# Optimization experiments

Hardware: AMD Instinct MI355X
Metric: run time of the kernel (lower is better)

## Reference

```python
import jax, jax.numpy as jnp
import numpy as np

DIM = 1024
HEADS = 16
DIM_HEAD = 64
INNER = HEADS * DIM_HEAD
B, N = 2, 2048


def rope_encoding(seq_len, dim_head):
    inv_freq = 1.0 / (10000.0 ** (jnp.arange(0, dim_head, 2, dtype=jnp.float32) / dim_head))
    pos = jnp.arange(seq_len, dtype=jnp.float32)
    sinusoid = pos[:, None] * inv_freq[None, :]          # [n, d/2]
    return jnp.concatenate([jnp.sin(sinusoid), jnp.cos(sinusoid)], axis=-1)  # [n, d]


def setup_inputs() -> dict:
    key = jax.random.key(0)
    k1, k2, k3, k4 = jax.random.split(key, 4)
    feats = jax.random.normal(k1, (B, N, DIM), dtype=jnp.float32)
    mask = jnp.ones((B, N), dtype=bool)
    # params (torch Linear: y = x @ W.T + b; store as [in, out] for x @ W)
    W_qkv = jax.random.normal(k2, (DIM, 3 * INNER), dtype=jnp.float32) / np.sqrt(DIM)
    W_out = jax.random.normal(k3, (INNER, DIM), dtype=jnp.float32) / np.sqrt(INNER)
    b_out = jax.random.normal(k4, (DIM,), dtype=jnp.float32) * 0.01
    return {"feats": feats, "W_qkv": W_qkv, "W_out": W_out, "b_out": b_out, "mask": mask}


def reference(feats, W_qkv, W_out, b_out, mask):
    b, n, _ = feats.shape
    h, d = HEADS, DIM_HEAD
    scale = d ** -0.5

    qkv = feats @ W_qkv                                   # [b, n, 3*inner]
    q, k, v = jnp.split(qkv, 3, axis=-1)
    to_bhnd = lambda t: t.reshape(b, n, h, d).transpose(0, 2, 1, 3)
    q, k, v = to_bhnd(q), to_bhnd(k), to_bhnd(v)          # [b, h, n, d]

    rope = rope_encoding(n, d)                            # [n, d]
    q = q + rope
    k = k + rope

    m = mask[:, None, :, None]                            # [b, 1, n, 1]
    neg_max = -jnp.finfo(k.dtype).max
    k = jnp.where(m, k, neg_max)

    q = jax.nn.softmax(q, axis=-1)                        # over feature dim
    k = jax.nn.softmax(k, axis=-2)                        # over sequence dim
    q = q * scale
    v = jnp.where(m, v, 0.0)

    context = jnp.einsum('bhnd,bhne->bhde', k, v)         # [b, h, d, d]
    out = jnp.einsum('bhde,bhnd->bhne', context, q)       # [b, h, n, d]
    out = out.transpose(0, 2, 1, 3).reshape(b, n, h * d)  # [b, n, inner]
    out = out @ W_out + b_out                             # [b, n, dim]

    attn = jnp.einsum('bhnd,bhmd->bhnm', q, k) * scale    # [b, h, n, n]
    return out, attn
```

## Files before the change

### kernel.cpp

```cpp
#include <hip/hip_runtime.h>
#include <cstddef>


#define BB     2
#define SEQ    2048
#define DIMM   1024
#define NHEADS 16
#define DH     64
#define TRIPLE 3072
#define ROWS   (BB*SEQ)
#define SCALE  0.125f

typedef unsigned short u16;
typedef unsigned int   u32;
typedef short s16x8 __attribute__((ext_vector_type(8)));
typedef float f32x4 __attribute__((ext_vector_type(4)));
typedef float vf4   __attribute__((ext_vector_type(4)));

static constexpr size_t WS_QB    = 0;
static constexpr size_t WS_KB    = 8388608;
static constexpr size_t WS_DEN   = 16777216;
static constexpr size_t WS_CTX   = 16785408;
static constexpr size_t WS_ROPET = 17309696;
static constexpr size_t WS_OPPK  = 17833984;
static constexpr size_t WS_WOPK  = 34611200;

static constexpr size_t SC_QKV  = 0;
static constexpr size_t SC_APK  = 50331648;
static constexpr size_t SC_WQPK = 67108864;

__device__ __forceinline__ u16 f2bf(float x) {
    u32 u = __float_as_uint(x);
    return (u16)((u + 0x7fffu + ((u >> 16) & 1u)) >> 16);
}
__device__ __forceinline__ float bf2f(u16 h) {
    return __uint_as_float(((u32)h) << 16);
}
__device__ __forceinline__ void glds16(const char* g, char* l) {
    __builtin_amdgcn_global_load_lds(
        (const __attribute__((address_space(1))) void*)g,
        (__attribute__((address_space(3))) void*)l, 16, 0, 0);
}

__device__ __forceinline__ void conv_pack_item(const float* __restrict__ src,
                                               u16* __restrict__ dst, int t)
{
    int g  = t & 3;
    int kb = (t >> 2) & 31;
    int row = t >> 7;
    const float* s = src + (size_t)row * 1024 + kb * 32 + 4 * g;
    float4 xa = *(const float4*)s;
    float4 xb = *(const float4*)(s + 16);
    float xs[8] = {xa.x, xa.y, xa.z, xa.w, xb.x, xb.y, xb.z, xb.w};
    s16x8 hv, lv;
    #pragma unroll
    for (int e = 0; e < 8; ++e) {
        u16 h = f2bf(xs[e]);
        hv[e] = (short)h;
        lv[e] = (short)f2bf(xs[e] - bf2f(h));
    }
    size_t rowc = (size_t)row * 256 + kb * 8;
    int sw = row & 7;
    *(s16x8*)(dst + (rowc + (size_t)(g ^ sw)) * 8)       = hv;
    *(s16x8*)(dst + (rowc + (size_t)((4 | g) ^ sw)) * 8) = lv;
}

__device__ __forceinline__ void conv_packT_tile(const float* __restrict__ W,
                                                u16* __restrict__ dst, int N,
                                                int n0, int kb, int t,
                                                float (*fb)[128])
{
    int k0 = kb * 32;
    #pragma unroll
    for (int q = 0; q < 4; ++q) {
        int cc = q * 256 + t;
        int kr = cc >> 5, nc = (cc & 31) * 4;
        *(float4*)&fb[kr][nc] = *(const float4*)&W[(size_t)(k0 + kr) * N + n0 + nc];
    }
    __syncthreads();
    #pragma unroll
    for (int it = 0; it < 2; ++it) {
        int item = it * 256 + t;
        int g = (item >> 7) & 3, n = item & 127;
        s16x8 hv, lv;
        #pragma unroll
        for (int e = 0; e < 4; ++e) {
            float x0 = fb[4 * g + e][n];
            float x1 = fb[16 + 4 * g + e][n];
            u16 h0 = f2bf(x0), h1 = f2bf(x1);
            hv[e]     = (short)h0;
            hv[e + 4] = (short)h1;
            lv[e]     = (short)f2bf(x0 - bf2f(h0));
            lv[e + 4] = (short)f2bf(x1 - bf2f(h1));
        }
        int row = n0 + n;
        size_t rowc = (size_t)row * 256 + kb * 8;
        int sw = row & 7;
        *(s16x8*)(dst + (rowc + (size_t)(g ^ sw)) * 8)       = hv;
        *(s16x8*)(dst + (rowc + (size_t)((4 | g) ^ sw)) * 8) = lv;
    }
}

__global__ __launch_bounds__(256)
void prologue(float4* __restrict__ denctx, float4* __restrict__ ropeT,
              const float* __restrict__ feats, u16* __restrict__ A_pk,
              const float* __restrict__ Wqkv, u16* __restrict__ Wq_pk,
              const float* __restrict__ Wout, u16* __restrict__ Wo_pk)
{
    __shared__ float fb[32][128];
    const int bid = blockIdx.x, tid = threadIdx.x;
    if (bid < 130) {
        denctx[bid * 256 + tid] = float4{0.f, 0.f, 0.f, 0.f};
        return;
    }
    if (bid < 258) {
        int t = (bid - 130) * 256 + tid;
        int pos = t >> 4, r16 = t & 15;
        double a0 = (double)pos * pow(10000.0, -(double)r16 / 32.0);
        double a1 = (double)pos * pow(10000.0, -(double)(r16 + 16) / 32.0);
        float4 v;
        v.x = (float)sin(a0); v.y = (float)sin(a1);
        v.z = (float)cos(a0); v.w = (float)cos(a1);
        ropeT[t] = v;
        return;
    }
    if (bid < 2306) {
        conv_pack_item(feats, A_pk, (bid - 258) * 256 + tid);
        return;
    }
    if (bid < 3074) {
        int cb = bid - 2306;
        conv_packT_tile(Wqkv, Wq_pk, TRIPLE, (cb % 24) * 128, cb / 24, tid, fb);
        return;
    }
    {
        int cb = bid - 3074;
        conv_packT_tile(Wout, Wo_pk, DIMM, (cb & 7) * 128, cb >> 3, tid, fb);
    }
}

__global__ __launch_bounds__(256, 3)
void gemm_qkv(const u16* __restrict__ Ap, const u16* __restrict__ Bp,
              float* __restrict__ C, const float* __restrict__ ropeT,
              float* __restrict__ den)
{
    __shared__ __align__(16) char smem[32768];
    const int tid = threadIdx.x;
    const int lane = tid & 63, wid = tid >> 6;
    const int wi = wid >> 1, wj = wid & 1;
    const int r16 = lane & 15, g = lane >> 4;

    const int bid = blockIdx.x;
    const int swz = (bid & 7) * 96 + (bid >> 3);
    const int bx = swz % 24, by = swz / 24;
    const int brow = by * 128, bcol = bx * 128;

    const int srow = wid * 32 + (lane >> 3);
    const int sch  = lane & 7;
    const char* gA = (const char*)Ap + ((size_t)(brow + srow) * 256 + sch) * 16;
    const char* gB = (const char*)Bp + ((size_t)(bcol + srow) * 256 + sch) * 16;
    char* la = smem + wid * 4096;
    char* lb = smem + 16384 + wid * 4096;

    f32x4 acc[4][4] = {};
    size_t koff = 0;
    for (int kb = 0; kb < 32; ++kb, koff += 128) {
        #pragma unroll
        for (int q = 0; q < 4; ++q) {
            glds16(gA + (size_t)q * (8 * 4096) + koff, la + q * 1024);
            glds16(gB + (size_t)q * (8 * 4096) + koff, lb + q * 1024);
        }
        __syncthreads();
        s16x8 ah[4], al[4], bh[4], bl[4];
        #pragma unroll
        for (int i = 0; i < 4; ++i) {
            int ra = wi * 64 + i * 16 + r16;
            const s16x8* Ar = (const s16x8*)(smem + (size_t)ra * 128);
            ah[i] = Ar[g ^ (ra & 7)];
            al[i] = Ar[(4 | g) ^ (ra & 7)];
            int rb = wj * 64 + i * 16 + r16;
            const s16x8* Br = (const s16x8*)(smem + 16384 + (size_t)rb * 128);
            bh[i] = Br[g ^ (rb & 7)];
            bl[i] = Br[(4 | g) ^ (rb & 7)];
        }
        #pragma unroll
        for (int i = 0; i < 4; ++i)
            #pragma unroll
            for (int j = 0; j < 4; ++j) {
                acc[i][j] = __builtin_amdgcn_mfma_f32_16x16x32_bf16(ah[i], bh[j], acc[i][j], 0, 0, 0);
                acc[i][j] = __builtin_amdgcn_mfma_f32_16x16x32_bf16(ah[i], bl[j], acc[i][j], 0, 0, 0);
                acc[i][j] = __builtin_amdgcn_mfma_f32_16x16x32_bf16(al[i], bh[j], acc[i][j], 0, 0, 0);
            }
        __syncthreads();
    }

    const int pos0 = brow & (SEQ - 1);
    const vf4* rT = (const vf4*)ropeT;
    if (bx < 8) {
        #pragma unroll
        for (int i = 0; i < 4; ++i)
            #pragma unroll
            for (int r = 0; r < 4; ++r) {
                int rloc = wi * 64 + i * 16 + g * 4 + r;
                vf4 rv = rT[(size_t)(pos0 + rloc) * 16 + r16];
                float v[4];
                #pragma unroll
                for (int j = 0; j < 4; ++j) v[j] = acc[i][j][r] + rv[j];
                float m = fmaxf(fmaxf(v[0], v[1]), fmaxf(v[2], v[3]));
                #pragma unroll
                for (int o = 1; o <= 8; o <<= 1) m = fmaxf(m, __shfl_xor(m, o));
                float e[4];
                float s = 0.f;
                #pragma unroll
                for (int j = 0; j < 4; ++j) { e[j] = expf(v[j] - m); s += e[j]; }
                #pragma unroll
                for (int o = 1; o <= 8; o <<= 1) s += __shfl_xor(s, o);
                float inv = SCALE / s;
                size_t rb = (size_t)(brow + rloc) * TRIPLE + bcol + wj * 64;
                #pragma unroll
                for (int j = 0; j < 4; ++j)
                    C[rb + j * 16 + r16] = e[j] * inv;
            }
    } else if (bx < 16) {
        float dsum[4] = {0.f, 0.f, 0.f, 0.f};
        #pragma unroll
        for (int i = 0; i < 4; ++i)
            #pragma unroll
            for (int r = 0; r < 4; ++r) {
                int rloc = wi * 64 + i * 16 + g * 4 + r;
                vf4 rv = rT[(size_t)(pos0 + rloc) * 16 + r16];
                size_t rb = (size_t)(brow + rloc) * TRIPLE + bcol + wj * 64;
                #pragma unroll
                for (int j = 0; j < 4; ++j) {
                    float e = expf(acc[i][j][r] + rv[j]);
                    C[rb + j * 16 + r16] = e;
                    dsum[j] += e;
                }
            }
        const int bD = (brow >> 11) * DIMM;
        #pragma unroll
        for (int j = 0; j < 4; ++j) {
            float s = dsum[j];
            s += __shfl_xor(s, 16);
            s += __shfl_xor(s, 32);
            if (g == 0)
                atomicAdd(&den[bD + (bcol - DIMM) + wj * 64 + j * 16 + r16], s);
        }
    } else {
        #pragma unroll
        for (int i = 0; i < 4; ++i) {
            int row = brow + wi * 64 + i * 16 + g * 4;
            #pragma unroll
            for (int j = 0; j < 4; ++j) {
                int col = bcol + wj * 64 + j * 16 + r16;
                #pragma unroll
                for (int r = 0; r < 4; ++r)
                    C[(size_t)(row + r) * TRIPLE + col] = acc[i][j][r];
            }
        }
    }
}

__global__ __launch_bounds__(256)
void packctx(const float* __restrict__ qkv, const float* __restrict__ den,
             u16* __restrict__ qb, u16* __restrict__ kb, float* __restrict__ ctx)
{
    __shared__ float kt[32][64];
    __shared__ float vt[32][64];
    if (blockIdx.x < 2048) {
        int t = blockIdx.x * 256 + threadIdx.x;
        int g  = t & 3;
        int db = (t >> 2) & 1;
        int h  = (t >> 3) & 15;
        int row = t >> 7;
        int b = row >> 11, n = row & (SEQ - 1);
        size_t dst = ((size_t)(b * NHEADS + h) * SEQ + n) * 64 + db * 32 + g * 8;
        const float* sq = qkv + (size_t)row * TRIPLE + h * DH + db * 32 + 4 * g;
        {
            float4 xa = *(const float4*)sq;
            float4 xb = *(const float4*)(sq + 16);
            float xs[8] = {xa.x, xa.y, xa.z, xa.w, xb.x, xb.y, xb.z, xb.w};
            s16x8 hv;
            #pragma unroll
            for (int e = 0; e < 8; ++e) hv[e] = (short)f2bf(xs[e]);
            *(s16x8*)(qb + dst) = hv;
        }
        {
            const float* sk = sq + DIMM;
            const float* dn = den + (size_t)b * DIMM + h * DH + db * 32 + 4 * g;
            float4 xa = *(const float4*)sk;
            float4 xb = *(const float4*)(sk + 16);
            float4 da = *(const float4*)dn;
            float4 dc = *(const float4*)(dn + 16);
            float xs[8] = {xa.x / da.x, xa.y / da.y, xa.z / da.z, xa.w / da.w,
                           xb.x / dc.x, xb.y / dc.y, xb.z / dc.z, xb.w / dc.w};
            s16x8 hv;
            #pragma unroll
            for (int e = 0; e < 8; ++e) hv[e] = (short)f2bf(xs[e]);
            *(s16x8*)(kb + dst) = hv;
        }
        return;
    }
    int cb = blockIdx.x - 2048;
    int chunk = cb & 7, h = (cb >> 3) & 15, b = cb >> 7;
    int row0 = b * SEQ + chunk * 256;
    int d  = threadIdx.x & 63;
    int eg = threadIdx.x >> 6;
    float acc[16] = {};
    for (int t = 0; t < 8; ++t) {
        #pragma unroll
        for (int q = 0; q < 2; ++q) {
            int lf = threadIdx.x * 2 + q;
            int nn = lf >> 4;
            int c4 = (lf & 15) * 4;
            size_t base = (size_t)(row0 + t * 32 + nn) * TRIPLE + DIMM + h * DH + c4;
            *(float4*)&kt[nn][c4] = *(const float4*)&qkv[base];
            *(float4*)&vt[nn][c4] = *(const float4*)&qkv[base + DIMM];
        }
        __syncthreads();
        #pragma unroll 8
        for (int nn = 0; nn < 32; ++nn) {
            float kv = kt[nn][d];
            #pragma unroll
            for (int j = 0; j < 16; ++j)
                acc[j] = fmaf(kv, vt[nn][eg * 16 + j], acc[j]);
        }
        __syncthreads();
    }
    float rden = 1.f / den[(size_t)b * DIMM + h * DH + d];
    size_t cbase = ((size_t)(b * NHEADS + h)) * (DH * DH) + d * DH + eg * 16;
    #pragma unroll
    for (int j = 0; j < 16; ++j) atomicAdd(&ctx[cbase + j], acc[j] * rden);
}

__global__ __launch_bounds__(256)
void outpre(const float* __restrict__ qkv, const float* __restrict__ ctx,
            u16* __restrict__ op_pk)
{
    int h = blockIdx.y, b = blockIdx.z;
    int row0 = b * SEQ + blockIdx.x * 64;
    __shared__ float cl[64][64];
    __shared__ float ql[4][64];
    const float* C = ctx + ((size_t)(b * NHEADS + h)) * (DH * DH);
    for (int i = threadIdx.x; i < DH * DH; i += 256) cl[i >> 6][i & 63] = C[i];
    __syncthreads();
    int w = threadIdx.x >> 6, lane = threadIdx.x & 63;
    const int m    = lane & 31;
    const int kbI  = h * 2 + (lane >> 5);
    const int g2   = (m & 15) >> 2;
    const int elem = (m & 3) | ((m >> 4) << 2);
    for (int it = 0; it < 16; ++it) {
        int row = row0 + w * 16 + it;
        float qv = qkv[(size_t)row * TRIPLE + h * DH + lane];
        ql[w][lane] = qv;
        float acc = 0.f;
        #pragma unroll
        for (int d = 0; d < 64; ++d) acc = fmaf(cl[d][lane], ql[w][d], acc);
        u16 hi = f2bf(acc);
        u16 lo = f2bf(acc - bf2f(hi));
        int sw = row & 7;
        size_t base = (size_t)row * 2048 + (size_t)kbI * 64;
        op_pk[base + ((g2 ^ sw) * 8 + elem)]       = hi;
        op_pk[base + (((4 | g2) ^ sw) * 8 + elem)] = lo;
    }
}

__global__ __launch_bounds__(256, 2)
void epilogue2(const u16* __restrict__ Op_pk, const u16* __restrict__ Wo_pk,
               float* __restrict__ outp, const float* __restrict__ bias,
               const u16* __restrict__ qb, const u16* __restrict__ kb,
               float* __restrict__ attn)
{
    __shared__ __align__(16) char smem[65536];
    const int tid = threadIdx.x;
    const int lane = tid & 63, wid = tid >> 6;
    const int r16 = lane & 15, g = lane >> 4;
    const int bid = blockIdx.x;

    if (bid % 17 == 0) {
        const int gb = bid / 17;
        const int wi = wid >> 1, wj = wid & 1;
        const int swz = (gb & 7) * 64 + (gb >> 3);
        const int bx = swz >> 6, by = swz & 63;
        const int brow = by * 64, bcol = bx * 128;
        const int srA = wid * 16 + (lane >> 3);
        const int srB = wid * 32 + (lane >> 3);
        const int sch = lane & 7;
        const char* gA = (const char*)Op_pk + ((size_t)(brow + srA) * 256 + sch) * 16;
        const char* gB = (const char*)Wo_pk + ((size_t)(bcol + srB) * 256 + sch) * 16;

        auto STAGE = [&](int buf, int kb2) {
            size_t koff = (size_t)kb2 * 128;
            char* a = smem + buf * 24576 + wid * 2048;
            char* b = smem + buf * 24576 + 8192 + wid * 4096;
            #pragma unroll
            for (int q = 0; q < 2; ++q)
                glds16(gA + (size_t)q * (8 * 4096) + koff, a + q * 1024);
            #pragma unroll
            for (int q = 0; q < 4; ++q)
                glds16(gB + (size_t)q * (8 * 4096) + koff, b + q * 1024);
        };

        f32x4 acc[2][4] = {};
        STAGE(0, 0);
        __syncthreads();
        for (int kb2 = 0; kb2 < 32; ++kb2) {
            const int cur = kb2 & 1;
            if (kb2 < 31) STAGE(cur ^ 1, kb2 + 1);
            const char* Ab = smem + cur * 24576;
            const char* Bb = smem + cur * 24576 + 8192;
            s16x8 ah[2], al[2], bh[4], bl[4];
            #pragma unroll
            for (int i = 0; i < 2; ++i) {
                int ra = wi * 32 + i * 16 + r16;
                const s16x8* Ar = (const s16x8*)(Ab + (size_t)ra * 128);
                ah[i] = Ar[g ^ (ra & 7)];
                al[i] = Ar[(4 | g) ^ (ra & 7)];
            }
            #pragma unroll
            for (int j = 0; j < 4; ++j) {
                int rb = wj * 64 + j * 16 + r16;
                const s16x8* Br = (const s16x8*)(Bb + (size_t)rb * 128);
                bh[j] = Br[g ^ (rb & 7)];
                bl[j] = Br[(4 | g) ^ (rb & 7)];
            }
            #pragma unroll
            for (int i = 0; i < 2; ++i)
                #pragma unroll
                for (int j = 0; j < 4; ++j) {
                    acc[i][j] = __builtin_amdgcn_mfma_f32_16x16x32_bf16(ah[i], bh[j], acc[i][j], 0, 0, 0);
                    acc[i][j] = __builtin_amdgcn_mfma_f32_16x16x32_bf16(ah[i], bl[j], acc[i][j], 0, 0, 0);
                    acc[i][j] = __builtin_amdgcn_mfma_f32_16x16x32_bf16(al[i], bh[j], acc[i][j], 0, 0, 0);
                }
            __syncthreads();
        }
        #pragma unroll
        for (int i = 0; i < 2; ++i) {
            int row = brow + wi * 32 + i * 16 + g * 4;
            #pragma unroll
            for (int j = 0; j < 4; ++j) {
                int col = bcol + wj * 64 + j * 16 + r16;
                float bv = bias[col];
                #pragma unroll
                for (int r = 0; r < 4; ++r)
                    outp[(size_t)(row + r) * DIMM + col] = acc[i][j][r] + bv;
            }
        }
        return;
    }

    const int ab = bid - bid / 17 - 1;
    const int bh = ab >> 8;
    const int n0 = ((ab >> 4) & 15) * 128, m0 = (ab & 15) * 128;
    const int wi = wid >> 1, wj = wid & 1;
    float* ost = (float*)smem;
    const u16* qB = qb + (size_t)bh * (SEQ * 64);
    const u16* kB = kb + (size_t)bh * (SEQ * 64);
    f32x4 acc[4][4] = {};
    #pragma unroll
    for (int db = 0; db < 2; ++db) {
        s16x8 a[4], b[4];
        #pragma unroll
        for (int i = 0; i < 4; ++i) {
            a[i] = *(const s16x8*)(qB + (size_t)(n0 + wi * 64 + i * 16 + r16) * 64 + db * 32 + g * 8);
            b[i] = *(const s16x8*)(kB + (size_t)(m0 + wj * 64 + i * 16 + r16) * 64 + db * 32 + g * 8);
        }
        #pragma unroll
        for (int i = 0; i < 4; ++i)
            #pragma unroll
            for (int j = 0; j < 4; ++j)
                acc[i][j] = __builtin_amdgcn_mfma_f32_16x16x32_bf16(a[i], b[j], acc[i][j], 0, 0, 0);
    }
    #pragma unroll
    for (int i = 0; i < 4; ++i)
        #pragma unroll
        for (int j = 0; j < 4; ++j)
            #pragma unroll
            for (int r = 0; r < 4; ++r)
                ost[(wi * 64 + i * 16 + g * 4 + r) * 128 + wj * 64 + j * 16 + r16] =
                    acc[i][j][r] * SCALE;
    __syncthreads();
    size_t base = (size_t)bh * ((size_t)SEQ * SEQ) + (size_t)n0 * SEQ + m0;
    int rr = tid >> 5, c16 = tid & 31;
    #pragma unroll
    for (int it = 0; it < 16; ++it) {
        int row = rr * 16 + it;
        vf4 v = *(vf4*)&ost[row * 128 + c16 * 4];
        __builtin_nontemporal_store(v, (vf4*)&attn[base + (size_t)row * SEQ + c16 * 4]);
    }
}

extern "C" void kernel_launch(void* const* d_in, const int* in_sizes, int n_in,
                              void* d_out, int out_size, void* d_ws, size_t ws_size,
                              hipStream_t stream)
{
    const float* feats = (const float*)d_in[0];
    const float* Wqkv  = (const float*)d_in[1];
    const float* Wout  = (const float*)d_in[2];
    const float* bout  = (const float*)d_in[3];

    char*  wsb   = (char*)d_ws;
    u16*   qb    = (u16*)(wsb + WS_QB);
    u16*   kb    = (u16*)(wsb + WS_KB);
    float* den   = (float*)(wsb + WS_DEN);
    float* ctx   = (float*)(wsb + WS_CTX);
    float* ropeT = (float*)(wsb + WS_ROPET);
    u16*   Op_pk = (u16*)(wsb + WS_OPPK);
    u16*   Wo_pk = (u16*)(wsb + WS_WOPK);

    float* out  = (float*)d_out;
    float* attn = out + (size_t)ROWS * DIMM;
    char*  sc   = (char*)attn;
    float* qkv   = (float*)(sc + SC_QKV);
    u16*   A_pk  = (u16*)(sc + SC_APK);
    u16*   Wq_pk = (u16*)(sc + SC_WQPK);

    prologue<<<3330, 256, 0, stream>>>((float4*)den, (float4*)ropeT,
                                       feats, A_pk, Wqkv, Wq_pk, Wout, Wo_pk);
    gemm_qkv<<<768, 256, 0, stream>>>(A_pk, Wq_pk, qkv, ropeT, den);
    packctx<<<2304, 256, 0, stream>>>(qkv, den, qb, kb, ctx);
    outpre<<<dim3(SEQ / 64, NHEADS, BB), 256, 0, stream>>>(qkv, ctx, Op_pk);
    epilogue2<<<8704, 256, 0, stream>>>(Op_pk, Wo_pk, out, bout, qb, kb, attn);
}
```

Measured before the change: 334.0 us.

## Fold per-head context into output weights instead of computing context-times-q per row

```diff
diff --git a/kernel.cpp b/kernel.cpp
--- a/kernel.cpp
+++ b/kernel.cpp
@@ -22,8 +22,8 @@
 static constexpr size_t WS_DEN   = 16777216;
 static constexpr size_t WS_CTX   = 16785408;
 static constexpr size_t WS_ROPET = 17309696;
-static constexpr size_t WS_OPPK  = 17833984;
-static constexpr size_t WS_WOPK  = 34611200;
+static constexpr size_t WS_AQPK  = 17833984;
+static constexpr size_t WS_W2PK  = 34611200;
 
 static constexpr size_t SC_QKV  = 0;
 static constexpr size_t SC_APK  = 50331648;
@@ -65,47 +65,10 @@
     *(s16x8*)(dst + (rowc + (size_t)((4 | g) ^ sw)) * 8) = lv;
 }
 
-__device__ __forceinline__ void conv_packT_tile(const float* __restrict__ W,
-                                                u16* __restrict__ dst, int N,
-                                                int n0, int kb, int t,
-                                                float (*fb)[128])
-{
-    int k0 = kb * 32;
-    #pragma unroll
-    for (int q = 0; q < 4; ++q) {
-        int cc = q * 256 + t;
-        int kr = cc >> 5, nc = (cc & 31) * 4;
-        *(float4*)&fb[kr][nc] = *(const float4*)&W[(size_t)(k0 + kr) * N + n0 + nc];
-    }
-    __syncthreads();
-    #pragma unroll
-    for (int it = 0; it < 2; ++it) {
-        int item = it * 256 + t;
-        int g = (item >> 7) & 3, n = item & 127;
-        s16x8 hv, lv;
-        #pragma unroll
-        for (int e = 0; e < 4; ++e) {
-            float x0 = fb[4 * g + e][n];
-            float x1 = fb[16 + 4 * g + e][n];
-            u16 h0 = f2bf(x0), h1 = f2bf(x1);
-            hv[e]     = (short)h0;
-            hv[e + 4] = (short)h1;
-            lv[e]     = (short)f2bf(x0 - bf2f(h0));
-            lv[e + 4] = (short)f2bf(x1 - bf2f(h1));
-        }
-        int row = n0 + n;
-        size_t rowc = (size_t)row * 256 + kb * 8;
-        int sw = row & 7;
-        *(s16x8*)(dst + (rowc + (size_t)(g ^ sw)) * 8)       = hv;
-        *(s16x8*)(dst + (rowc + (size_t)((4 | g) ^ sw)) * 8) = lv;
-    }
-}
-
 __global__ __launch_bounds__(256)
 void prologue(float4* __restrict__ denctx, float4* __restrict__ ropeT,
               const float* __restrict__ feats, u16* __restrict__ A_pk,
-              const float* __restrict__ Wqkv, u16* __restrict__ Wq_pk,
-              const float* __restrict__ Wout, u16* __restrict__ Wo_pk)
+              const float* __restrict__ Wqkv, u16* __restrict__ Wq_pk)
 {
     __shared__ float fb[32][128];
     const int bid = blockIdx.x, tid = threadIdx.x;
@@ -128,14 +91,37 @@
         conv_pack_item(feats, A_pk, (bid - 258) * 256 + tid);
         return;
     }
-    if (bid < 3074) {
+    {
         int cb = bid - 2306;
-        conv_packT_tile(Wqkv, Wq_pk, TRIPLE, (cb % 24) * 128, cb / 24, tid, fb);
-        return;
-    }
-    {
-        int cb = bid - 3074;
-        conv_packT_tile(Wout, Wo_pk, DIMM, (cb & 7) * 128, cb >> 3, tid, fb);
+        int n0 = (cb % 24) * 128, kb = cb / 24, k0 = kb * 32;
+        #pragma unroll
+        for (int q = 0; q < 4; ++q) {
+            int cc = q * 256 + tid;
+            int kr = cc >> 5, nc = (cc & 31) * 4;
+            *(float4*)&fb[kr][nc] = *(const float4*)&Wqkv[(size_t)(k0 + kr) * TRIPLE + n0 + nc];
+        }
+        __syncthreads();
+        #pragma unroll
+        for (int it = 0; it < 2; ++it) {
+            int item = it * 256 + tid;
+            int g = (item >> 7) & 3, n = item & 127;
+            s16x8 hv, lv;
+            #pragma unroll
+            for (int e = 0; e < 4; ++e) {
+                float x0 = fb[4 * g + e][n];
+                float x1 = fb[16 + 4 * g + e][n];
+                u16 h0 = f2bf(x0), h1 = f2bf(x1);
+                hv[e]     = (short)h0;
+                hv[e + 4] = (short)h1;
+                lv[e]     = (short)f2bf(x0 - bf2f(h0));
+                lv[e + 4] = (short)f2bf(x1 - bf2f(h1));
+            }
+            int row = n0 + n;
+            size_t rowc = (size_t)row * 256 + kb * 8;
+            int sw = row & 7;
+            *(s16x8*)(Wq_pk + (rowc + (size_t)(g ^ sw)) * 8)       = hv;
+            *(s16x8*)(Wq_pk + (rowc + (size_t)((4 | g) ^ sw)) * 8) = lv;
+        }
     }
 }
 
@@ -263,7 +249,8 @@
 
 __global__ __launch_bounds__(256)
 void packctx(const float* __restrict__ qkv, const float* __restrict__ den,
-             u16* __restrict__ qb, u16* __restrict__ kb, float* __restrict__ ctx)
+             u16* __restrict__ qb, u16* __restrict__ kb,
+             u16* __restrict__ Aq_pk, float* __restrict__ ctx)
 {
     __shared__ float kt[32][64];
     __shared__ float vt[32][64];
@@ -280,10 +267,18 @@
             float4 xa = *(const float4*)sq;
             float4 xb = *(const float4*)(sq + 16);
             float xs[8] = {xa.x, xa.y, xa.z, xa.w, xb.x, xb.y, xb.z, xb.w};
-            s16x8 hv;
-            #pragma unroll
-            for (int e = 0; e < 8; ++e) hv[e] = (short)f2bf(xs[e]);
+            s16x8 hv, lv;
+            #pragma unroll
+            for (int e = 0; e < 8; ++e) {
+                u16 hh = f2bf(xs[e]);
+                hv[e] = (short)hh;
+                lv[e] = (short)f2bf(xs[e] - bf2f(hh));
+            }
             *(s16x8*)(qb + dst) = hv;
+            int sw = row & 7;
+            size_t base = (size_t)row * 2048 + (size_t)(h * 2 + db) * 64;
+            *(s16x8*)(Aq_pk + base + (size_t)((g ^ sw) * 8))       = hv;
+            *(s16x8*)(Aq_pk + base + (size_t)((((4 | g) ^ sw)) * 8)) = lv;
         }
         {
             const float* sk = sq + DIMM;
@@ -334,44 +329,49 @@
 }
 
 __global__ __launch_bounds__(256)
-void outpre(const float* __restrict__ qkv, const float* __restrict__ ctx,
-            u16* __restrict__ op_pk)
-{
-    int h = blockIdx.y, b = blockIdx.z;
-    int row0 = b * SEQ + blockIdx.x * 64;
+void W2k(const float* __restrict__ ctx, const float* __restrict__ Wout,
+         u16* __restrict__ W2_pk)
+{
     __shared__ float cl[64][64];
-    __shared__ float ql[4][64];
+    const int bid = blockIdx.x, tid = threadIdx.x;
+    const int ct = bid & 7, h = (bid >> 3) & 15, b = bid >> 7;
     const float* C = ctx + ((size_t)(b * NHEADS + h)) * (DH * DH);
-    for (int i = threadIdx.x; i < DH * DH; i += 256) cl[i >> 6][i & 63] = C[i];
+    for (int i = tid; i < DH * DH; i += 256) cl[i >> 6][i & 63] = C[i];
     __syncthreads();
-    int w = threadIdx.x >> 6, lane = threadIdx.x & 63;
-    const int m    = lane & 31;
-    const int kbI  = h * 2 + (lane >> 5);
-    const int g2   = (m & 15) >> 2;
-    const int elem = (m & 3) | ((m >> 4) << 2);
-    for (int it = 0; it < 16; ++it) {
-        int row = row0 + w * 16 + it;
-        float qv = qkv[(size_t)row * TRIPLE + h * DH + lane];
-        ql[w][lane] = qv;
-        float acc = 0.f;
-        #pragma unroll
-        for (int d = 0; d < 64; ++d) acc = fmaf(cl[d][lane], ql[w][d], acc);
-        u16 hi = f2bf(acc);
-        u16 lo = f2bf(acc - bf2f(hi));
-        int sw = row & 7;
-        size_t base = (size_t)row * 2048 + (size_t)kbI * 64;
-        op_pk[base + ((g2 ^ sw) * 8 + elem)]       = hi;
-        op_pk[base + (((4 | g2) ^ sw) * 8 + elem)] = lo;
-    }
-}
-
-__global__ __launch_bounds__(256, 2)
-void epilogue2(const u16* __restrict__ Op_pk, const u16* __restrict__ Wo_pk,
+    const int c = ct * 128 + (tid & 127);
+    const int dg = tid >> 7;
+    float acc[32] = {};
+    for (int e = 0; e < 64; ++e) {
+        float wv = Wout[(size_t)(h * 64 + e) * DIMM + c];
+        #pragma unroll
+        for (int r = 0; r < 32; ++r)
+            acc[r] = fmaf(cl[dg * 32 + r][e], wv, acc[r]);
+    }
+    s16x8 hv[4], lv[4];
+    #pragma unroll
+    for (int r = 0; r < 32; ++r) {
+        int g2 = (r & 15) >> 2;
+        int elem = (r & 3) + 4 * (r >> 4);
+        u16 hh = f2bf(acc[r]);
+        hv[g2][elem] = (short)hh;
+        lv[g2][elem] = (short)f2bf(acc[r] - bf2f(hh));
+    }
+    const int sw = c & 7;
+    u16* base = W2_pk + (size_t)b * 2097152 + (size_t)c * 2048 + (size_t)(h * 2 + dg) * 64;
+    #pragma unroll
+    for (int g2 = 0; g2 < 4; ++g2) {
+        *(s16x8*)(base + ((g2 ^ sw) * 8))       = hv[g2];
+        *(s16x8*)(base + (((4 | g2) ^ sw) * 8)) = lv[g2];
+    }
+}
+
+__global__ __launch_bounds__(256, 3)
+void epilogue2(const u16* __restrict__ Aq_pk, const u16* __restrict__ W2_pk,
                float* __restrict__ outp, const float* __restrict__ bias,
                const u16* __restrict__ qb, const u16* __restrict__ kb,
                float* __restrict__ attn)
 {
-    __shared__ __align__(16) char smem[65536];
+    __shared__ __align__(16) char smem[49152];
     const int tid = threadIdx.x;
     const int lane = tid & 63, wid = tid >> 6;
     const int r16 = lane & 15, g = lane >> 4;
@@ -386,8 +386,9 @@
         const int srA = wid * 16 + (lane >> 3);
         const int srB = wid * 32 + (lane >> 3);
         const int sch = lane & 7;
-        const char* gA = (const char*)Op_pk + ((size_t)(brow + srA) * 256 + sch) * 16;
-        const char* gB = (const char*)Wo_pk + ((size_t)(bcol + srB) * 256 + sch) * 16;
+        const char* gA = (const char*)Aq_pk + ((size_t)(brow + srA) * 256 + sch) * 16;
+        const char* gB = (const char*)(W2_pk + (size_t)(brow >> 11) * 2097152)
+                         + ((size_t)(bcol + srB) * 256 + sch) * 16;
 
         auto STAGE = [&](int buf, int kb2) {
             size_t koff = (size_t)kb2 * 128;
@@ -453,7 +454,6 @@
     const int bh = ab >> 8;
     const int n0 = ((ab >> 4) & 15) * 128, m0 = (ab & 15) * 128;
     const int wi = wid >> 1, wj = wid & 1;
-    float* ost = (float*)smem;
     const u16* qB = qb + (size_t)bh * (SEQ * 64);
     const u16* kB = kb + (size_t)bh * (SEQ * 64);
     f32x4 acc[4][4] = {};
@@ -471,22 +471,16 @@
             for (int j = 0; j < 4; ++j)
                 acc[i][j] = __builtin_amdgcn_mfma_f32_16x16x32_bf16(a[i], b[j], acc[i][j], 0, 0, 0);
     }
+    size_t base = (size_t)bh * ((size_t)SEQ * SEQ);
     #pragma unroll
-    for (int i = 0; i < 4; ++i)
-        #pragma unroll
-        for (int j = 0; j < 4; ++j)
-            #pragma unroll
-            for (int r = 0; r < 4; ++r)
-                ost[(wi * 64 + i * 16 + g * 4 + r) * 128 + wj * 64 + j * 16 + r16] =
-                    acc[i][j][r] * SCALE;
-    __syncthreads();
-    size_t base = (size_t)bh * ((size_t)SEQ * SEQ) + (size_t)n0 * SEQ + m0;
-    int rr = tid >> 5, c16 = tid & 31;
-    #pragma unroll
-    for (int it = 0; it < 16; ++it) {
-        int row = rr * 16 + it;
-        vf4 v = *(vf4*)&ost[row * 128 + c16 * 4];
-        __builtin_nontemporal_store(v, (vf4*)&attn[base + (size_t)row * SEQ + c16 * 4]);
+    for (int i = 0; i < 4; ++i) {
+        #pragma unroll
+        for (int r = 0; r < 4; ++r) {
+            size_t rowb = base + (size_t)(n0 + wi * 64 + i * 16 + g * 4 + r) * SEQ + m0 + wj * 64 + r16;
+            #pragma unroll
+            for (int j = 0; j < 4; ++j)
+                __builtin_nontemporal_store(acc[i][j][r] * SCALE, &attn[rowb + j * 16]);
+        }
     }
 }
 
@@ -505,8 +499,8 @@
     float* den   = (float*)(wsb + WS_DEN);
     float* ctx   = (float*)(wsb + WS_CTX);
     float* ropeT = (float*)(wsb + WS_ROPET);
-    u16*   Op_pk = (u16*)(wsb + WS_OPPK);
-    u16*   Wo_pk = (u16*)(wsb + WS_WOPK);
+    u16*   Aq_pk = (u16*)(wsb + WS_AQPK);
+    u16*   W2_pk = (u16*)(wsb + WS_W2PK);
 
     float* out  = (float*)d_out;
     float* attn = out + (size_t)ROWS * DIMM;
@@ -515,10 +509,10 @@
     u16*   A_pk  = (u16*)(sc + SC_APK);
     u16*   Wq_pk = (u16*)(sc + SC_WQPK);
 
-    prologue<<<3330, 256, 0, stream>>>((float4*)den, (float4*)ropeT,
-                                       feats, A_pk, Wqkv, Wq_pk, Wout, Wo_pk);
+    prologue<<<3074, 256, 0, stream>>>((float4*)den, (float4*)ropeT,
+                                       feats, A_pk, Wqkv, Wq_pk);
     gemm_qkv<<<768, 256, 0, stream>>>(A_pk, Wq_pk, qkv, ropeT, den);
-    packctx<<<2304, 256, 0, stream>>>(qkv, den, qb, kb, ctx);
-    outpre<<<dim3(SEQ / 64, NHEADS, BB), 256, 0, stream>>>(qkv, ctx, Op_pk);
-    epilogue2<<<8704, 256, 0, stream>>>(Op_pk, Wo_pk, out, bout, qb, kb, attn);
-}
+    packctx<<<2304, 256, 0, stream>>>(qkv, den, qb, kb, Aq_pk, ctx);
+    W2k<<<256, 256, 0, stream>>>(ctx, Wout, W2_pk);
+    epilogue2<<<8704, 256, 0, stream>>>(Aq_pk, W2_pk, out, bout, qb, kb, attn);
+}
```

Measured after the change: 359.0 us. 1.07x slower.
